# Performance work log

Measured on AMD Instinct MI355X. Metric: run time of the kernel, lower is better.

## Reference

```python
import jax, jax.numpy as jnp
import numpy as np

NHEAD = 8  # nn.MultiheadAttention default in TransformerDecoderLayerOptimal
LN_EPS = 1e-5


def layer_norm(x, g, b):
    m = x.mean(-1, keepdims=True)
    v = ((x - m) ** 2).mean(-1, keepdims=True)
    return (x - m) * jax.lax.rsqrt(v + LN_EPS) * g + b


def setup_inputs() -> dict:
    key = jax.random.key(0)
    ks = jax.random.split(key, 16)
    B, S, F0, D, L, C, DF = 32, 1024, 2048, 768, 100, 1000, 10
    sc = 0.02
    return {
        "x": jax.random.normal(ks[0], (B, S, F0), jnp.float32),
        "y": jax.random.normal(ks[1], (L, D), jnp.float32),
        "embed_W": jax.random.normal(ks[2], (D, F0), jnp.float32) * sc,
        "embed_b": jnp.zeros((D,), jnp.float32),
        "Wq": jax.random.normal(ks[3], (D, D), jnp.float32) * sc,
        "Wk": jax.random.normal(ks[4], (D, D), jnp.float32) * sc,
        "Wv": jax.random.normal(ks[5], (D, D), jnp.float32) * sc,
        "bq": jnp.zeros((D,), jnp.float32),
        "bk": jnp.zeros((D,), jnp.float32),
        "bv": jnp.zeros((D,), jnp.float32),
        "Wo": jax.random.normal(ks[6], (D, D), jnp.float32) * sc,
        "bo": jnp.zeros((D,), jnp.float32),
        "ln1_g": jnp.ones((D,), jnp.float32), "ln1_b": jnp.zeros((D,), jnp.float32),
        "ln2_g": jnp.ones((D,), jnp.float32), "ln2_b": jnp.zeros((D,), jnp.float32),
        "ln3_g": jnp.ones((D,), jnp.float32), "ln3_b": jnp.zeros((D,), jnp.float32),
        "ffn_W1": jax.random.normal(ks[7], (D, D), jnp.float32) * sc,  # dim_feedforward = d_model
        "ffn_b1": jnp.zeros((D,), jnp.float32),
        "ffn_W2": jax.random.normal(ks[8], (D, D), jnp.float32) * sc,
        "ffn_b2": jnp.zeros((D,), jnp.float32),
        "dup_pool": jax.random.normal(ks[9], (L, 2 * D, DF), jnp.float32) * sc,
        "dup_bias": jnp.zeros((C,), jnp.float32),
    }


def reference(x, y, embed_W, embed_b, Wq, Wk, Wv, bq, bk, bv, Wo, bo,
              ln1_g, ln1_b, ln2_g, ln2_b, ln3_g, ln3_b,
              ffn_W1, ffn_b1, ffn_W2, ffn_b2, dup_pool, dup_bias):
    B = x.shape[0]
    L, D = y.shape
    H, hd = NHEAD, D // NHEAD
    num_classes = dup_bias.shape[0]

    # embed_standart + relu : (B,S,F0) -> (B,S,D)
    mem = jax.nn.relu(jnp.einsum('bsf,df->bsd', x, embed_W) + embed_b)

    # tgt = query_embed repeated over batch (batch-first here)
    tgt0 = jnp.broadcast_to(y[None], (B, L, D))

    # TransformerDecoderLayerOptimal (eval mode: dropout = identity)
    t = layer_norm(tgt0 + tgt0, ln1_g, ln1_b)  # tgt + dropout1(tgt)

    # cross multi-head attention
    q = (jnp.einsum('bld,ed->ble', t, Wq) + bq).reshape(B, L, H, hd)
    k = (jnp.einsum('bsd,ed->bse', mem, Wk) + bk).reshape(B, -1, H, hd)
    v = (jnp.einsum('bsd,ed->bse', mem, Wv) + bv).reshape(B, -1, H, hd)
    scores = jnp.einsum('blhe,bshe->bhls', q, k) / np.float32(np.sqrt(hd))
    attn = jax.nn.softmax(scores, axis=-1)           # (B,H,L,S)
    ao = jnp.einsum('bhls,bshe->blhe', attn, v).reshape(B, L, D)
    ao = jnp.einsum('bld,ed->ble', ao, Wo) + bo
    t = layer_norm(t + ao, ln2_g, ln2_b)

    # FFN
    f = jnp.einsum('bld,ed->ble',
                   jax.nn.relu(jnp.einsum('bld,ed->ble', t, ffn_W1) + ffn_b1),
                   ffn_W2) + ffn_b2
    h = layer_norm(t + f, ln3_g, ln3_b)              # (B,L,D)

    # concat label embedding after h, then GroupFC (per-label grouped matmul)
    hcat = jnp.concatenate([h, tgt0], axis=-1)       # (B,L,2D)
    out_extrap = jnp.einsum('bld,ldf->blf', hcat, dup_pool)  # (B,L,DF)
    logits = out_extrap.reshape(B, -1)[:, :num_classes] + dup_bias

    a_score = attn.mean(axis=1)                      # MHA averages heads: (B,L,S)
    return logits, a_score
```

## Files before the change

kernel.cpp:

```cpp
#include <hip/hip_runtime.h>

typedef unsigned short u16;
typedef __bf16 bf16x8 __attribute__((ext_vector_type(8)));
typedef short s16x8 __attribute__((ext_vector_type(8)));
typedef u16 u16x4 __attribute__((ext_vector_type(4)));
typedef float f32x4 __attribute__((ext_vector_type(4)));

__device__ __forceinline__ float b2f(u16 u) {
  union { unsigned u32; float f; } x; x.u32 = ((unsigned)u) << 16; return x.f;
}
__device__ __forceinline__ u16 f2b(float f) {
  return __builtin_bit_cast(u16, (__bf16)f);
}
__device__ __forceinline__ s16x8 cvt8(f32x4 a, f32x4 b) {
  s16x8 r;
#pragma unroll
  for (int i = 0; i < 4; ++i) {
    r[i]     = (short)f2b(a[i]);
    r[i + 4] = (short)f2b(b[i]);
  }
  return r;
}

template <int F32>
__device__ __forceinline__ s16x8 load8(const void* __restrict__ p, size_t idx) {
  if (F32) {
    const float* f = (const float*)p + idx;
    return cvt8(*(const f32x4*)f, *(const f32x4*)(f + 4));
  } else {
    return *(const s16x8*)((const u16*)p + idx);
  }
}

__device__ __forceinline__ void gl16(const u16* g, u16* l) {
  __builtin_amdgcn_global_load_lds(
      (const __attribute__((address_space(1))) void*)g,
      (__attribute__((address_space(3))) void*)l, 16, 0, 0);
}

__global__ __launch_bounds__(256) void cvt_kernel(const float* __restrict__ in,
                                                  u16* __restrict__ out, int n8) {
  int i = blockIdx.x * 256 + threadIdx.x;
  if (i < n8) *(s16x8*)&out[(size_t)i * 8] = load8<1>(in, (size_t)i * 8);
}

__global__ __launch_bounds__(256) void cvt3_kernel(
    const float* __restrict__ a, const float* __restrict__ b,
    const float* __restrict__ c, u16* __restrict__ oa, u16* __restrict__ ob,
    u16* __restrict__ oc, int n8) {
  int i = blockIdx.x * 256 + threadIdx.x;
  const float* in = blockIdx.y == 0 ? a : (blockIdx.y == 1 ? b : c);
  u16* out = blockIdx.y == 0 ? oa : (blockIdx.y == 1 ? ob : oc);
  if (i < n8) *(s16x8*)&out[(size_t)i * 8] = load8<1>(in, (size_t)i * 8);
}

template <int RELU, int AF32, int TRANSC, int BM>
__global__ __launch_bounds__(2 * BM) void gemm_bt_kernel(
    const void* __restrict__ A, const u16* __restrict__ Bt,
    const float* __restrict__ bias, u16* __restrict__ C,
    int M, int N, int K) {
  __shared__ u16 As[2][BM][32];
  __shared__ u16 Bs[2][128][32];
  const int tid = threadIdx.x;
  const int lane = tid & 63;
  const int wave = tid >> 6;
  const int wm = wave >> 1, wn = wave & 1;
  const int nwg = gridDim.x;
  const int orig = blockIdx.x;
  const int q = nwg >> 3, r = nwg & 7;
  const int xcd = orig & 7, loc = orig >> 3;
  const int wgid = (xcd < r ? xcd * (q + 1) : r * (q + 1) + (xcd - r) * q) + loc;
  const int NT = N >> 7;
  const int tn = wgid % NT, tm = wgid / NT;
  const size_t abase = (size_t)tm * BM * K;
  const size_t bbase = (size_t)tn * 128 * K;
  const int fr = lane & 15;
  const int fk = (lane >> 4) << 3;
  const int grow = lane >> 2;
  const int gkoff = (lane & 3) << 3;
  const int browB = (BM == 256) ? wave * 16 : wave * 32;
  const u16* bgp = Bt + bbase + (size_t)(browB + grow) * K + gkoff;
  const u16* agp = (const u16*)A + abase + (size_t)(wave * 32 + grow) * K + gkoff;
  const int lr = tid >> 2;
  const int lk = (tid & 3) << 3;
  const float* afp  = (const float*)A + abase + (size_t)lr * K + lk;
  const float* afp2 = afp + (size_t)(BM / 2) * K;
  const int nk = K >> 5;
  f32x4 acc[4][4] = {};
  f32x4 p0, p1, p2, p3;

  if (AF32) {
    p0 = *(const f32x4*)afp;  p1 = *(const f32x4*)(afp + 4);
    p2 = *(const f32x4*)afp2; p3 = *(const f32x4*)(afp2 + 4);
    *(s16x8*)&As[0][lr][lk]          = cvt8(p0, p1);
    *(s16x8*)&As[0][lr + BM / 2][lk] = cvt8(p2, p3);
    const int k1 = (nk > 1) ? 32 : 0;
    p0 = *(const f32x4*)(afp + k1);  p1 = *(const f32x4*)(afp + k1 + 4);
    p2 = *(const f32x4*)(afp2 + k1); p3 = *(const f32x4*)(afp2 + k1 + 4);
  } else {
    gl16(agp, &As[0][wave * 32][0]);
    gl16(agp + (size_t)16 * K, &As[0][wave * 32 + 16][0]);
  }
  gl16(bgp, &Bs[0][browB][0]);
  if (BM == 128) gl16(bgp + (size_t)16 * K, &Bs[0][browB + 16][0]);

  int c = 0;
  for (int t = 0; t < nk; ++t) {
    const int nb = c ^ 1;
    if (t + 1 < nk) {
      if (AF32) {
        *(s16x8*)&As[nb][lr][lk]          = cvt8(p0, p1);
        *(s16x8*)&As[nb][lr + BM / 2][lk] = cvt8(p2, p3);
        const int k2 = ((t + 2 < nk) ? (t + 2) : (nk - 1)) << 5;
        p0 = *(const f32x4*)(afp + k2);  p1 = *(const f32x4*)(afp + k2 + 4);
        p2 = *(const f32x4*)(afp2 + k2); p3 = *(const f32x4*)(afp2 + k2 + 4);
      } else {
        gl16(agp + (t + 1) * 32, &As[nb][wave * 32][0]);
        gl16(agp + (t + 1) * 32 + (size_t)16 * K, &As[nb][wave * 32 + 16][0]);
      }
      gl16(bgp + (t + 1) * 32, &Bs[nb][browB][0]);
      if (BM == 128) gl16(bgp + (t + 1) * 32 + (size_t)16 * K, &Bs[nb][browB + 16][0]);
    }
    __builtin_amdgcn_sched_barrier(0);
    if (t + 1 < nk) {
      asm volatile("s_waitcnt vmcnt(%0)" ::"n"(
          AF32 ? (BM == 256 ? 5 : 6) : (BM == 256 ? 3 : 4)) : "memory");
    } else {
      asm volatile("s_waitcnt vmcnt(0)" ::: "memory");
    }
    if (AF32) asm volatile("s_waitcnt lgkmcnt(0)" ::: "memory");
    __builtin_amdgcn_sched_barrier(0);
    __builtin_amdgcn_s_barrier();
    __builtin_amdgcn_sched_barrier(0);

    bf16x8 af[4], bfv[4];
#pragma unroll
    for (int i = 0; i < 4; ++i)
      af[i] = __builtin_bit_cast(bf16x8, *(const s16x8*)&As[c][wm * 64 + i * 16 + fr][fk]);
#pragma unroll
    for (int j = 0; j < 4; ++j)
      bfv[j] = __builtin_bit_cast(bf16x8, *(const s16x8*)&Bs[c][wn * 64 + j * 16 + fr][fk]);
#pragma unroll
    for (int i = 0; i < 4; ++i)
#pragma unroll
      for (int j = 0; j < 4; ++j)
        acc[i][j] = __builtin_amdgcn_mfma_f32_16x16x32_bf16(af[i], bfv[j], acc[i][j], 0, 0, 0);
    __builtin_amdgcn_s_barrier();
    c = nb;
  }

  const int row0 = tm * BM + wm * 64 + ((lane >> 4) << 2);
  const int col0 = tn * 128 + wn * 64 + fr;
  if (TRANSC) {
#pragma unroll
    for (int j = 0; j < 4; ++j) {
      const int col = col0 + j * 16;
      const float bv = bias[col];
#pragma unroll
      for (int i = 0; i < 4; ++i) {
        const int row = row0 + i * 16;
        u16x4 pk;
#pragma unroll
        for (int r2 = 0; r2 < 4; ++r2) {
          float v = acc[i][j][r2] + bv;
          if (RELU) v = fmaxf(v, 0.f);
          pk[r2] = f2b(v);
        }
        size_t idx = ((size_t)(row >> 10) * N + col) * 1024 + (row & 1023);
        *(u16x4*)&C[idx] = pk;
      }
    }
  } else {
#pragma unroll
    for (int j = 0; j < 4; ++j) {
      const int col = col0 + j * 16;
      const float bv = bias[col];
#pragma unroll
      for (int i = 0; i < 4; ++i) {
#pragma unroll
        for (int r2 = 0; r2 < 4; ++r2) {
          float v = acc[i][j][r2] + bv;
          if (RELU) v = fmaxf(v, 0.f);
          C[(size_t)(row0 + i * 16 + r2) * N + col] = f2b(v);
        }
      }
    }
  }
}

__device__ __forceinline__ void block_stats(float s, float s2, float* red, int tid,
                                            float& S, float& S2) {
#pragma unroll
  for (int o = 32; o > 0; o >>= 1) { s += __shfl_xor(s, o); s2 += __shfl_xor(s2, o); }
  if ((tid & 63) == 0) { red[tid >> 6] = s; red[4 + (tid >> 6)] = s2; }
  __syncthreads();
  S = red[0] + red[1] + red[2] + red[3];
  S2 = red[4] + red[5] + red[6] + red[7];
}

__global__ __launch_bounds__(256) void t_kernel(const float* __restrict__ y,
                                                const float* __restrict__ g,
                                                const float* __restrict__ bb,
                                                float* __restrict__ t) {
  const int l = blockIdx.x, tid = threadIdx.x;
  __shared__ float red[8];
  float xv[3], s = 0.f, s2 = 0.f;
#pragma unroll
  for (int i = 0; i < 3; ++i) {
    int e = tid + i * 256;
    float v = 2.f * y[(size_t)l * 768 + e];
    xv[i] = v; s += v; s2 += v * v;
  }
  float S, S2;
  block_stats(s, s2, red, tid, S, S2);
  float mean = S * (1.f / 768.f);
  float var = S2 * (1.f / 768.f) - mean * mean;
  float inv = rsqrtf(var + 1e-5f);
#pragma unroll
  for (int i = 0; i < 3; ++i) {
    int e = tid + i * 256;
    t[(size_t)l * 768 + e] = (xv[i] - mean) * inv * g[e] + bb[e];
  }
}

__global__ __launch_bounds__(256) void q_kernel(const float* __restrict__ t,
                                                const float* __restrict__ Wq,
                                                const float* __restrict__ bq,
                                                float* __restrict__ q) {
  const int l = blockIdx.x, tid = threadIdx.x;
  __shared__ __align__(16) float ts[768];
  for (int i = tid; i < 768; i += 256) ts[i] = t[(size_t)l * 768 + i];
  __syncthreads();
  for (int e = tid; e < 768; e += 256) {
    const float* wr = Wq + (size_t)e * 768;
    float acc = bq[e];
    for (int j = 0; j < 768; j += 4) {
      f32x4 wv = *(const f32x4*)&wr[j];
      f32x4 tv = *(const f32x4*)&ts[j];
      acc += wv[0] * tv[0] + wv[1] * tv[1] + wv[2] * tv[2] + wv[3] * tv[3];
    }
    q[(size_t)l * 768 + e] = acc;
  }
}

__global__ __launch_bounds__(256) void c2_kernel(const float* __restrict__ y,
                                                 const float* __restrict__ pool,
                                                 const float* __restrict__ dbias,
                                                 float* __restrict__ c2) {
  const int l = blockIdx.x, tid = threadIdx.x, lane = tid & 63, w = tid >> 6;
  for (int j = w; j < 10; j += 4) {
    float acc = 0.f;
    for (int d = lane; d < 768; d += 64)
      acc += y[(size_t)l * 768 + d] * pool[((size_t)l * 1536 + 768 + d) * 10 + j];
#pragma unroll
    for (int o = 32; o > 0; o >>= 1) acc += __shfl_xor(acc, o);
    if (lane == 0) c2[l * 10 + j] = acc + dbias[l * 10 + j];
  }
}

__global__ __launch_bounds__(512) void attn_kernel(
    const float* __restrict__ q,
    const u16* __restrict__ kmat,
    const u16* __restrict__ vt,
    u16* __restrict__ ao,
    float* __restrict__ ascore) {
  const int b = blockIdx.x;
  const int l0 = blockIdx.y * 13;
  __shared__ float sc[13][1028];
  __shared__ __align__(16) u16 qs[16][96];
  __shared__ float rinv[16];
  const int tid = threadIdx.x;
  const int lane = tid & 63;
  const int w = tid >> 6;
  const int fr = lane & 15;
  const int hi = lane >> 4;
  const int fk = hi << 3;
  const int sfr = (fr < 13) ? fr : 12;
  float areg[26];
#pragma unroll
  for (int j = 0; j < 26; ++j) areg[j] = 0.f;

  for (int h = 0; h < 8; ++h) {
    for (int i = tid; i < 192; i += 512) {
      int r = i / 12, c8 = (i % 12) * 8;
      int l = l0 + r;
      s16x8 v = {};
      if (r < 13 && l < 100) v = load8<1>(q, (size_t)l * 768 + h * 96 + c8);
      *(s16x8*)&qs[r][c8] = v;
    }
    __syncthreads();
    bf16x8 af[3];
#pragma unroll
    for (int kk = 0; kk < 3; ++kk)
      af[kk] = __builtin_bit_cast(bf16x8, *(const s16x8*)&qs[fr][kk * 32 + fk]);
    const u16* kbase = kmat + (size_t)(b * 1024 + w * 128 + fr) * 768 + h * 96 + fk;
#pragma unroll 2
    for (int nt = 0; nt < 8; ++nt) {
      f32x4 acc = {};
      const u16* kp = kbase + (size_t)nt * 16 * 768;
#pragma unroll
      for (int kk = 0; kk < 3; ++kk) {
        bf16x8 bf = __builtin_bit_cast(bf16x8, *(const s16x8*)(kp + kk * 32));
        acc = __builtin_amdgcn_mfma_f32_16x16x32_bf16(af[kk], bf, acc, 0, 0, 0);
      }
      const int s = w * 128 + nt * 16 + fr;
#pragma unroll
      for (int r = 0; r < 4; ++r) {
        int lr2 = hi * 4 + r;
        if (lr2 < 13) sc[lr2][s] = acc[r] * 0.10206207261596575f;
      }
    }
    __syncthreads();
    for (int r = w; r < 13; r += 8) {
      float m = -1e30f;
      for (int i = lane; i < 1024; i += 64) m = fmaxf(m, sc[r][i]);
#pragma unroll
      for (int o = 32; o > 0; o >>= 1) m = fmaxf(m, __shfl_xor(m, o));
      float sum = 0.f;
      for (int i = lane; i < 1024; i += 64) {
        float e = __expf(sc[r][i] - m);
        sc[r][i] = e; sum += e;
      }
#pragma unroll
      for (int o = 32; o > 0; o >>= 1) sum += __shfl_xor(sum, o);
      if (lane == 0) rinv[r] = 1.f / sum;
    }
    __syncthreads();
#pragma unroll
    for (int j = 0; j < 26; ++j) {
      int i = tid + j * 512;
      int r = i >> 10;
      areg[j] += sc[r][i & 1023] * rinv[r];
    }
    f32x4 pacc[6];
#pragma unroll
    for (int nt = 0; nt < 6; ++nt) pacc[nt] = (f32x4){0.f, 0.f, 0.f, 0.f};
    const u16* vbase = vt + (size_t)(b * 768 + h * 96 + fr) * 1024 + w * 128 + fk;
#pragma unroll 2
    for (int ks = 0; ks < 4; ++ks) {
      const float* sp = &sc[sfr][w * 128 + ks * 32 + fk];
      bf16x8 paf;
#pragma unroll
      for (int j2 = 0; j2 < 8; ++j2) paf[j2] = (__bf16)sp[j2];
#pragma unroll
      for (int nt = 0; nt < 6; ++nt) {
        bf16x8 vf = __builtin_bit_cast(bf16x8,
            *(const s16x8*)(vbase + (size_t)nt * 16 * 1024 + ks * 32));
        pacc[nt] = __builtin_amdgcn_mfma_f32_16x16x32_bf16(paf, vf, pacc[nt], 0, 0, 0);
      }
    }
    __syncthreads();
    float* red = &sc[0][0];
#pragma unroll
    for (int nt = 0; nt < 6; ++nt) {
#pragma unroll
      for (int r = 0; r < 4; ++r) {
        int lr2 = hi * 4 + r;
        if (lr2 < 13) red[(w * 13 + lr2) * 96 + nt * 16 + fr] = pacc[nt][r];
      }
    }
    __syncthreads();
    for (int i = tid; i < 1248; i += 512) {
      int lr2 = i / 96, d = i % 96;
      float s = 0.f;
#pragma unroll
      for (int w8 = 0; w8 < 8; ++w8) s += red[(w8 * 13 + lr2) * 96 + d];
      int l = l0 + lr2;
      if (l < 100) ao[(size_t)(b * 100 + l) * 768 + h * 96 + d] = f2b(s * rinv[lr2]);
    }
    __syncthreads();
  }
#pragma unroll
  for (int j = 0; j < 26; ++j) {
    int i = tid + j * 512;
    int r = i >> 10;
    int l = l0 + r;
    if (l < 100) ascore[(size_t)(b * 100 + l) * 1024 + (i & 1023)] = areg[j] * 0.125f;
  }
}

__global__ __launch_bounds__(256) void ln_kernel(
    const float* __restrict__ base, const u16* __restrict__ add,
    const float* __restrict__ g, const float* __restrict__ bb,
    float* __restrict__ outf, u16* __restrict__ outb, int base_per_l) {
  const int row = blockIdx.x, tid = threadIdx.x;
  __shared__ float red[8];
  const size_t boff = (size_t)(base_per_l ? (row % 100) : row) * 768;
  const size_t aoff = (size_t)row * 768;
  float xv[3], s = 0.f, s2 = 0.f;
#pragma unroll
  for (int i = 0; i < 3; ++i) {
    int e = tid + i * 256;
    float v = base[boff + e] + b2f(add[aoff + e]);
    xv[i] = v; s += v; s2 += v * v;
  }
  float S, S2;
  block_stats(s, s2, red, tid, S, S2);
  float mean = S * (1.f / 768.f);
  float var = S2 * (1.f / 768.f) - mean * mean;
  float inv = rsqrtf(var + 1e-5f);
#pragma unroll
  for (int i = 0; i < 3; ++i) {
    int e = tid + i * 256;
    float o = (xv[i] - mean) * inv * g[e] + bb[e];
    if (outf) outf[aoff + e] = o;
    if (outb) outb[aoff + e] = f2b(o);
  }
}

__global__ __launch_bounds__(256) void groupfc_kernel(
    const u16* __restrict__ h, const float* __restrict__ pool,
    const float* __restrict__ c2, float* __restrict__ logits) {
  const int l = blockIdx.x, tid = threadIdx.x;
  __shared__ float ps[768][10];
  for (int i = tid; i < 7680; i += 256) ps[i / 10][i % 10] = pool[(size_t)l * 15360 + i];
  __syncthreads();
  for (int idx = tid; idx < 320; idx += 256) {
    int bb = idx / 10, j = idx % 10;
    const u16* hr = h + (size_t)(bb * 100 + l) * 768;
    float acc = c2[l * 10 + j];
    for (int d0 = 0; d0 < 768; d0 += 8) {
      s16x8 hv = *(const s16x8*)&hr[d0];
#pragma unroll
      for (int e = 0; e < 8; ++e) acc += b2f((u16)hv[e]) * ps[d0 + e][j];
    }
    logits[bb * 1000 + l * 10 + j] = acc;
  }
}

extern "C" void kernel_launch(void* const* d_in, const int* in_sizes, int n_in,
                              void* d_out, int out_size, void* d_ws, size_t ws_size,
                              hipStream_t stream) {
  (void)in_sizes; (void)n_in; (void)out_size; (void)ws_size;
  const float* x      = (const float*)d_in[0];
  const float* y      = (const float*)d_in[1];
  const float* embedW = (const float*)d_in[2];
  const float* embedb = (const float*)d_in[3];
  const float* Wq     = (const float*)d_in[4];
  const float* Wk     = (const float*)d_in[5];
  const float* Wv     = (const float*)d_in[6];
  const float* bq     = (const float*)d_in[7];
  const float* bk     = (const float*)d_in[8];
  const float* bv     = (const float*)d_in[9];
  const float* Wo     = (const float*)d_in[10];
  const float* bo     = (const float*)d_in[11];
  const float* ln1g   = (const float*)d_in[12];
  const float* ln1b   = (const float*)d_in[13];
  const float* ln2g   = (const float*)d_in[14];
  const float* ln2b   = (const float*)d_in[15];
  const float* ln3g   = (const float*)d_in[16];
  const float* ln3b   = (const float*)d_in[17];
  const float* W1     = (const float*)d_in[18];
  const float* b1     = (const float*)d_in[19];
  const float* W2     = (const float*)d_in[20];
  const float* b2     = (const float*)d_in[21];
  const float* pool   = (const float*)d_in[22];
  const float* dbias  = (const float*)d_in[23];

  char* w = (char*)d_ws;
  u16* kws = (u16*)(w);
  u16* vt  = (u16*)(w + 50331648);
  char* R  = w + 100663296;
  u16*   mem = (u16*)R;
  u16*   ao  = (u16*)(R + 0);
  u16*   u1  = (u16*)(R + 4915200);
  u16*   t2b = (u16*)(R + 9830400);
  u16*   f1  = (u16*)(R + 14745600);
  u16*   f2  = (u16*)(R + 19660800);
  u16*   hb  = (u16*)(R + 24576000);
  float* t2f = (float*)(R + 29491200);
  float* tf  = (float*)(w + 150994944);
  float* qf  = (float*)(w + 150994944 + 307200);
  float* c2  = (float*)(w + 150994944 + 614400);
  u16* wbE = (u16*)(w + 50331648);
  u16* wbK = (u16*)(w + 50331648 + 3145728);
  u16* wbV = (u16*)(w + 150994944 + 1048576);
  u16* wbO = (u16*)(w + 0);
  u16* wb1 = (u16*)(w + 1179648);
  u16* wb2 = (u16*)(w + 2359296);

  float* logits = (float*)d_out;
  float* ascore = (float*)d_out + 32000;

  cvt_kernel<<<dim3(768), dim3(256), 0, stream>>>(embedW, wbE, 196608);
  cvt_kernel<<<dim3(288), dim3(256), 0, stream>>>(Wk, wbK, 73728);
  cvt_kernel<<<dim3(288), dim3(256), 0, stream>>>(Wv, wbV, 73728);
  t_kernel<<<dim3(100), dim3(256), 0, stream>>>(y, ln1g, ln1b, tf);
  q_kernel<<<dim3(100), dim3(256), 0, stream>>>(tf, Wq, bq, qf);
  c2_kernel<<<dim3(100), dim3(256), 0, stream>>>(y, pool, dbias, c2);

  gemm_bt_kernel<1, 1, 0, 256><<<dim3(768), dim3(512), 0, stream>>>(x, wbE, embedb, mem, 32768, 768, 2048);
  gemm_bt_kernel<0, 0, 0, 256><<<dim3(768), dim3(512), 0, stream>>>(mem, wbK, bk, kws, 32768, 768, 768);
  gemm_bt_kernel<0, 0, 1, 256><<<dim3(768), dim3(512), 0, stream>>>(mem, wbV, bv, vt, 32768, 768, 768);

  attn_kernel<<<dim3(32, 8), dim3(512), 0, stream>>>(qf, kws, vt, ao, ascore);

  cvt3_kernel<<<dim3(288, 3), dim3(256), 0, stream>>>(Wo, W1, W2, wbO, wb1, wb2, 73728);
  gemm_bt_kernel<0, 0, 0, 128><<<dim3(150), dim3(256), 0, stream>>>(ao, wbO, bo, u1, 3200, 768, 768);
  ln_kernel<<<dim3(3200), dim3(256), 0, stream>>>(tf, u1, ln2g, ln2b, t2f, t2b, 1);
  gemm_bt_kernel<1, 0, 0, 128><<<dim3(150), dim3(256), 0, stream>>>(t2b, wb1, b1, f1, 3200, 768, 768);
  gemm_bt_kernel<0, 0, 0, 128><<<dim3(150), dim3(256), 0, stream>>>(f1, wb2, b2, f2, 3200, 768, 768);
  ln_kernel<<<dim3(3200), dim3(256), 0, stream>>>(t2f, f2, ln3g, ln3b, (float*)nullptr, hb, 0);
  groupfc_kernel<<<dim3(100), dim3(256), 0, stream>>>(hb, pool, c2, logits);
}
```

Baseline: 995.3 us.

## Fuse K and V projections into a dual-output GEMM and shrink tile heights

Adds a DUAL mode to the bf16 GEMM. One launch computes both the K projection (row-major output) and the V projection (transposed output) from a single staged copy of the A tile, so the memory activations are read once instead of twice. The LDS B tile loading is generalised to any BM. The embed GEMM now uses BM=128 and the small decoder GEMMs use BM=64, giving more workgroups for the 3200-row problems at the cost of less A/B reuse per tile. The K weight copy is stored in the scratch area of the output buffer that the attention kernel overwrites later, and the dual kernel carries twice the accumulator registers, which may lower occupancy.

```diff
diff --git a/kernel.cpp b/kernel.cpp
--- a/kernel.cpp
+++ b/kernel.cpp
@@ -54,13 +54,18 @@
   if (i < n8) *(s16x8*)&out[(size_t)i * 8] = load8<1>(in, (size_t)i * 8);
 }
 
-template <int RELU, int AF32, int TRANSC, int BM>
+template <int RELU, int AF32, int TRANSC, int BM, int DUAL>
 __global__ __launch_bounds__(2 * BM) void gemm_bt_kernel(
     const void* __restrict__ A, const u16* __restrict__ Bt,
     const float* __restrict__ bias, u16* __restrict__ C,
-    int M, int N, int K) {
+    const u16* __restrict__ Bt2, const float* __restrict__ bias2,
+    u16* __restrict__ C2, int M, int N, int K) {
+  constexpr int NWAVE = BM / 32;
+  constexpr int NBG = 256 / BM;
+  constexpr int VPRE = (AF32 ? 4 : 2) + NBG * (DUAL ? 2 : 1);
   __shared__ u16 As[2][BM][32];
   __shared__ u16 Bs[2][128][32];
+  __shared__ u16 Bs2[DUAL ? 2 : 1][DUAL ? 128 : 1][32];
   const int tid = threadIdx.x;
   const int lane = tid & 63;
   const int wave = tid >> 6;
@@ -78,8 +83,9 @@
   const int fk = (lane >> 4) << 3;
   const int grow = lane >> 2;
   const int gkoff = (lane & 3) << 3;
-  const int browB = (BM == 256) ? wave * 16 : wave * 32;
+  const int browB = wave * (128 / NWAVE);
   const u16* bgp = Bt + bbase + (size_t)(browB + grow) * K + gkoff;
+  const u16* b2gp = Bt2 ? (Bt2 + bbase + (size_t)(browB + grow) * K + gkoff) : nullptr;
   const u16* agp = (const u16*)A + abase + (size_t)(wave * 32 + grow) * K + gkoff;
   const int lr = tid >> 2;
   const int lk = (tid & 3) << 3;
@@ -87,6 +93,7 @@
   const float* afp2 = afp + (size_t)(BM / 2) * K;
   const int nk = K >> 5;
   f32x4 acc[4][4] = {};
+  f32x4 acc2[4][4] = {};
   f32x4 p0, p1, p2, p3;
 
   if (AF32) {
@@ -101,8 +108,14 @@
     gl16(agp, &As[0][wave * 32][0]);
     gl16(agp + (size_t)16 * K, &As[0][wave * 32 + 16][0]);
   }
-  gl16(bgp, &Bs[0][browB][0]);
-  if (BM == 128) gl16(bgp + (size_t)16 * K, &Bs[0][browB + 16][0]);
+#pragma unroll
+  for (int bi = 0; bi < NBG; ++bi)
+    gl16(bgp + (size_t)(bi * 16) * K, &Bs[0][browB + bi * 16][0]);
+  if constexpr (DUAL) {
+#pragma unroll
+    for (int bi = 0; bi < NBG; ++bi)
+      gl16(b2gp + (size_t)(bi * 16) * K, &Bs2[0][browB + bi * 16][0]);
+  }
 
   int c = 0;
   for (int t = 0; t < nk; ++t) {
@@ -118,13 +131,18 @@
         gl16(agp + (t + 1) * 32, &As[nb][wave * 32][0]);
         gl16(agp + (t + 1) * 32 + (size_t)16 * K, &As[nb][wave * 32 + 16][0]);
       }
-      gl16(bgp + (t + 1) * 32, &Bs[nb][browB][0]);
-      if (BM == 128) gl16(bgp + (t + 1) * 32 + (size_t)16 * K, &Bs[nb][browB + 16][0]);
+#pragma unroll
+      for (int bi = 0; bi < NBG; ++bi)
+        gl16(bgp + (t + 1) * 32 + (size_t)(bi * 16) * K, &Bs[nb][browB + bi * 16][0]);
+      if constexpr (DUAL) {
+#pragma unroll
+        for (int bi = 0; bi < NBG; ++bi)
+          gl16(b2gp + (t + 1) * 32 + (size_t)(bi * 16) * K, &Bs2[nb][browB + bi * 16][0]);
+      }
     }
     __builtin_amdgcn_sched_barrier(0);
     if (t + 1 < nk) {
-      asm volatile("s_waitcnt vmcnt(%0)" ::"n"(
-          AF32 ? (BM == 256 ? 5 : 6) : (BM == 256 ? 3 : 4)) : "memory");
+      asm volatile("s_waitcnt vmcnt(%0)" ::"n"(VPRE) : "memory");
     } else {
       asm volatile("s_waitcnt vmcnt(0)" ::: "memory");
     }
@@ -133,25 +151,52 @@
     __builtin_amdgcn_s_barrier();
     __builtin_amdgcn_sched_barrier(0);
 
-    bf16x8 af[4], bfv[4];
+    bf16x8 af[4], bfv[4], bfv2[4];
 #pragma unroll
     for (int i = 0; i < 4; ++i)
       af[i] = __builtin_bit_cast(bf16x8, *(const s16x8*)&As[c][wm * 64 + i * 16 + fr][fk]);
 #pragma unroll
     for (int j = 0; j < 4; ++j)
       bfv[j] = __builtin_bit_cast(bf16x8, *(const s16x8*)&Bs[c][wn * 64 + j * 16 + fr][fk]);
+    if constexpr (DUAL) {
+#pragma unroll
+      for (int j = 0; j < 4; ++j)
+        bfv2[j] = __builtin_bit_cast(bf16x8, *(const s16x8*)&Bs2[c][wn * 64 + j * 16 + fr][fk]);
+    }
 #pragma unroll
     for (int i = 0; i < 4; ++i)
 #pragma unroll
-      for (int j = 0; j < 4; ++j)
+      for (int j = 0; j < 4; ++j) {
         acc[i][j] = __builtin_amdgcn_mfma_f32_16x16x32_bf16(af[i], bfv[j], acc[i][j], 0, 0, 0);
+        if constexpr (DUAL)
+          acc2[i][j] = __builtin_amdgcn_mfma_f32_16x16x32_bf16(af[i], bfv2[j], acc2[i][j], 0, 0, 0);
+      }
     __builtin_amdgcn_s_barrier();
     c = nb;
   }
 
   const int row0 = tm * BM + wm * 64 + ((lane >> 4) << 2);
   const int col0 = tn * 128 + wn * 64 + fr;
-  if (TRANSC) {
+  if constexpr (DUAL) {
+#pragma unroll
+    for (int j = 0; j < 4; ++j) {
+      const int col = col0 + j * 16;
+      const float bv = bias[col];
+      const float bv2 = bias2[col];
+#pragma unroll
+      for (int i = 0; i < 4; ++i) {
+        const int row = row0 + i * 16;
+        u16x4 pk;
+#pragma unroll
+        for (int r2 = 0; r2 < 4; ++r2) {
+          C[(size_t)(row + r2) * N + col] = f2b(acc[i][j][r2] + bv);
+          pk[r2] = f2b(acc2[i][j][r2] + bv2);
+        }
+        size_t idx = ((size_t)(row >> 10) * N + col) * 1024 + (row & 1023);
+        *(u16x4*)&C2[idx] = pk;
+      }
+    }
+  } else if constexpr (TRANSC) {
 #pragma unroll
     for (int j = 0; j < 4; ++j) {
       const int col = col0 + j * 16;
@@ -167,7 +212,7 @@
           pk[r2] = f2b(v);
         }
         size_t idx = ((size_t)(row >> 10) * N + col) * 1024 + (row & 1023);
-        *(u16x4*)&C[idx] = pk;
+        *(u16x4*)&C2[idx] = pk;
       }
     }
   } else {
@@ -473,8 +518,8 @@
   float* qf  = (float*)(w + 150994944 + 307200);
   float* c2  = (float*)(w + 150994944 + 614400);
   u16* wbE = (u16*)(w + 50331648);
-  u16* wbK = (u16*)(w + 50331648 + 3145728);
   u16* wbV = (u16*)(w + 150994944 + 1048576);
+  u16* wbK = (u16*)((char*)d_out + 128000);
   u16* wbO = (u16*)(w + 0);
   u16* wb1 = (u16*)(w + 1179648);
   u16* wb2 = (u16*)(w + 2359296);
@@ -489,17 +534,21 @@
   q_kernel<<<dim3(100), dim3(256), 0, stream>>>(tf, Wq, bq, qf);
   c2_kernel<<<dim3(100), dim3(256), 0, stream>>>(y, pool, dbias, c2);
 
-  gemm_bt_kernel<1, 1, 0, 256><<<dim3(768), dim3(512), 0, stream>>>(x, wbE, embedb, mem, 32768, 768, 2048);
-  gemm_bt_kernel<0, 0, 0, 256><<<dim3(768), dim3(512), 0, stream>>>(mem, wbK, bk, kws, 32768, 768, 768);
-  gemm_bt_kernel<0, 0, 1, 256><<<dim3(768), dim3(512), 0, stream>>>(mem, wbV, bv, vt, 32768, 768, 768);
+  gemm_bt_kernel<1, 1, 0, 128, 0><<<dim3(1536), dim3(256), 0, stream>>>(
+      x, wbE, embedb, mem, nullptr, nullptr, nullptr, 32768, 768, 2048);
+  gemm_bt_kernel<0, 0, 1, 128, 1><<<dim3(1536), dim3(256), 0, stream>>>(
+      mem, wbK, bk, kws, wbV, bv, vt, 32768, 768, 768);
 
   attn_kernel<<<dim3(32, 8), dim3(512), 0, stream>>>(qf, kws, vt, ao, ascore);
 
   cvt3_kernel<<<dim3(288, 3), dim3(256), 0, stream>>>(Wo, W1, W2, wbO, wb1, wb2, 73728);
-  gemm_bt_kernel<0, 0, 0, 128><<<dim3(150), dim3(256), 0, stream>>>(ao, wbO, bo, u1, 3200, 768, 768);
+  gemm_bt_kernel<0, 0, 0, 64, 0><<<dim3(300), dim3(128), 0, stream>>>(
+      ao, wbO, bo, u1, nullptr, nullptr, nullptr, 3200, 768, 768);
   ln_kernel<<<dim3(3200), dim3(256), 0, stream>>>(tf, u1, ln2g, ln2b, t2f, t2b, 1);
-  gemm_bt_kernel<1, 0, 0, 128><<<dim3(150), dim3(256), 0, stream>>>(t2b, wb1, b1, f1, 3200, 768, 768);
-  gemm_bt_kernel<0, 0, 0, 128><<<dim3(150), dim3(256), 0, stream>>>(f1, wb2, b2, f2, 3200, 768, 768);
+  gemm_bt_kernel<1, 0, 0, 64, 0><<<dim3(300), dim3(128), 0, stream>>>(
+      t2b, wb1, b1, f1, nullptr, nullptr, nullptr, 3200, 768, 768);
+  gemm_bt_kernel<0, 0, 0, 64, 0><<<dim3(300), dim3(128), 0, stream>>>(
+      f1, wb2, b2, f2, nullptr, nullptr, nullptr, 3200, 768, 768);
   ln_kernel<<<dim3(3200), dim3(256), 0, stream>>>(t2f, f2, ln3g, ln3b, (float*)nullptr, hb, 0);
   groupfc_kernel<<<dim3(100), dim3(256), 0, stream>>>(hb, pool, c2, logits);
 }
```

Result: slower. 1.017 ms (+2.2%).
